# Kernel optimization log

Measured on AMD Instinct MI355X. Metric: run time of the kernel, lower is better.

The kernel has to match this reference:

```python
import jax, jax.numpy as jnp
import numpy as np
import math

B, T, D_MOTION = 2, 1536, 256
D_MODEL, N_HEADS, D_FF, N_LAYERS = 512, 8, 2048, 6
D_HEAD = D_MODEL // N_HEADS
FPS = 30
PERIOD = FPS // 2
CONTEXT_FRAMES = 10
NEG = -1e9  # large negative instead of -inf so fully-masked rows give uniform attn, not NaN


def _w(k, shape, fan_in):
    return jax.random.normal(k, shape, jnp.float32) / np.sqrt(fan_in)


def setup_inputs() -> dict:
    key = jax.random.key(0)
    ks = jax.random.split(key, 16)
    L = N_LAYERS
    din = D_MOTION + 5 + 1
    inp = {
        'motion': jax.random.normal(ks[0], (B, T, D_MOTION), jnp.float32),
        'traj': jax.random.normal(ks[1], (B, T, 5), jnp.float32),
        'me_w1': _w(ks[2], (din, D_MODEL), din), 'me_b1': jnp.zeros((D_MODEL,), jnp.float32),
        'me_w2': _w(ks[3], (D_MODEL, D_MODEL), D_MODEL), 'me_b2': jnp.zeros((D_MODEL,), jnp.float32),
        'wq': _w(ks[4], (L, D_MODEL, D_MODEL), D_MODEL), 'bq': jnp.zeros((L, D_MODEL), jnp.float32),
        'wk': _w(ks[5], (L, D_MODEL, D_MODEL), D_MODEL), 'bk': jnp.zeros((L, D_MODEL), jnp.float32),
        'wv': _w(ks[6], (L, D_MODEL, D_MODEL), D_MODEL), 'bv': jnp.zeros((L, D_MODEL), jnp.float32),
        'wo': _w(ks[7], (L, D_MODEL, D_MODEL), D_MODEL), 'bo': jnp.zeros((L, D_MODEL), jnp.float32),
        'ln1_g': jnp.ones((L, D_MODEL), jnp.float32), 'ln1_b': jnp.zeros((L, D_MODEL), jnp.float32),
        'ffn_w1': _w(ks[8], (L, D_MODEL, D_FF), D_MODEL), 'ffn_b1': jnp.zeros((L, D_FF), jnp.float32),
        'ffn_w2': _w(ks[9], (L, D_FF, D_MODEL), D_FF), 'ffn_b2': jnp.zeros((L, D_MODEL), jnp.float32),
        'ln2_g': jnp.ones((L, D_MODEL), jnp.float32), 'ln2_b': jnp.zeros((L, D_MODEL), jnp.float32),
        'fln_g': jnp.ones((D_MODEL,), jnp.float32), 'fln_b': jnp.zeros((D_MODEL,), jnp.float32),
        'dec_w1': _w(ks[10], (D_MODEL, D_MODEL), D_MODEL), 'dec_b1': jnp.zeros((D_MODEL,), jnp.float32),
        'dec_w2': _w(ks[11], (D_MODEL, D_MOTION), D_MODEL), 'dec_b2': jnp.zeros((D_MOTION,), jnp.float32),
    }
    return inp


def _layer_norm(x, g, b):
    m = jnp.mean(x, axis=-1, keepdims=True)
    v = jnp.mean((x - m) ** 2, axis=-1, keepdims=True)
    return (x - m) * jax.lax.rsqrt(v + 1e-5) * g + b


def _leaky(x):
    return jnp.where(x >= 0, x, 0.01 * x)


def _forward(motion, traj, me_w1, me_b1, me_w2, me_b2, wq, bq, wk, bk, wv, bv, wo, bo,
             ln1_g, ln1_b, ffn_w1, ffn_b1, ffn_w2, ffn_b2, ln2_g, ln2_b,
             fln_g, fln_b, dec_w1, dec_b1, dec_w2, dec_b2):
    idx = jnp.arange(T)
    dist = jnp.abs(idx[:, None] - idx[None, :])                       # [T,T]
    atten_bias = -(dist // PERIOD).astype(jnp.float32)                # periodic distance bias

    # context mask: keep first context_frames and last frame
    batch_mask = jnp.ones((T, 1), jnp.float32).at[CONTEXT_FRAMES:-1].set(0.0)
    mask = jnp.broadcast_to(batch_mask[None], (B, T, 1))              # [B,T,1]
    cf = jnp.ones((T,), bool).at[CONTEXT_FRAMES:-1].set(False)        # constrained frames

    original_motion = motion
    motion = motion * mask

    # motion encoder (dropout inactive at eval)
    h = jnp.concatenate([motion, traj, mask], axis=-1)                # [B,T,D_MOTION+6]
    x = _leaky(h @ me_w1 + me_b1)
    x = _leaky(x @ me_w2 + me_b2)

    # periodic positional embedding (sinusoidal on pos mod period)
    pos = jnp.mod(jnp.arange(T, dtype=jnp.float32), float(PERIOD))
    half = D_MODEL // 2
    div = jnp.exp(-np.log(10000.0) * (2.0 * jnp.arange(half, dtype=jnp.float32)) / D_MODEL)
    ang = pos[:, None] * div[None, :]
    pe = jnp.concatenate([jnp.sin(ang), jnp.cos(ang)], axis=-1)       # [T,D_MODEL]
    x = x + pe[None]

    # dynamically growing attention window
    num_trans = T - CONTEXT_FRAMES - 1
    ksz = math.ceil(num_trans / 2 / N_LAYERS) * 2 + 1
    kern = jnp.ones((ksz,), jnp.float32)
    thr = ksz // 2
    scale = 1.0 / np.sqrt(D_HEAD)

    for i in range(N_LAYERS):
        # attn mask: True = blocked
        amask = (dist > thr) | (~cf)[None, :]                         # [T,T]
        h = _layer_norm(x, ln1_g[i], ln1_b[i])                        # pre-layernorm
        q = (h @ wq[i] + bq[i]).reshape(B, T, N_HEADS, D_HEAD)
        k = (h @ wk[i] + bk[i]).reshape(B, T, N_HEADS, D_HEAD)
        v = (h @ wv[i] + bv[i]).reshape(B, T, N_HEADS, D_HEAD)
        scores = jnp.einsum('bqhd,bkhd->bhqk', q, k) * scale + atten_bias
        scores = jnp.where(amask[None, None], NEG, scores)
        attn = jax.nn.softmax(scores, axis=-1)
        out = jnp.einsum('bhqk,bkhd->bqhd', attn, v).reshape(B, T, D_MODEL)
        x = x + out @ wo[i] + bo[i]
        # position-wise FFN (pre-layernorm)
        h = _layer_norm(x, ln2_g[i], ln2_b[i])
        x = x + jax.nn.relu(h @ ffn_w1[i] + ffn_b1[i]) @ ffn_w2[i] + ffn_b2[i]
        # grow constrained frames by conv1d with ones kernel (same padding)
        cf = jnp.convolve(cf.astype(jnp.float32), kern, mode='same') > 0.5

    x = _layer_norm(x, fln_g, fln_b)
    x = _leaky(x @ dec_w1 + dec_b1)
    x = x @ dec_w2 + dec_b2                                           # [B,T,D_MOTION]
    out = original_motion * mask + x * (1.0 - mask)
    return out, mask


def reference(motion, traj, me_w1, me_b1, me_w2, me_b2, wq, bq, wk, bk, wv, bv, wo, bo,
              ln1_g, ln1_b, ffn_w1, ffn_b1, ffn_w2, ffn_b2, ln2_g, ln2_b,
              fln_g, fln_b, dec_w1, dec_b1, dec_w2, dec_b2):
    return _forward(motion, traj, me_w1, me_b1, me_w2, me_b2, wq, bq, wk, bk, wv, bv, wo, bo,
                    ln1_g, ln1_b, ffn_w1, ffn_b1, ffn_w2, ffn_b2, ln2_g, ln2_b,
                    fln_g, fln_b, dec_w1, dec_b1, dec_w2, dec_b2)
```

## Files before the change

### kernel.cpp

```cpp
#include <hip/hip_runtime.h>
#include <math.h>

typedef unsigned short ushort_t;
typedef unsigned int uint_t;
typedef __bf16 bf16x4 __attribute__((ext_vector_type(4)));
typedef __bf16 bf16x8 __attribute__((ext_vector_type(8)));
typedef float f32x4 __attribute__((ext_vector_type(4)));

#define T_SEQ   1536
#define NB      2
#define MROWS   3072
#define DMODEL  512
#define NHEADS  8
#define DHEAD   64
#define DFF     2048
#define DMOTION 256
#define NLAYERS 6
#define PERIODN 15
#define CTXF    10
#define THRW    128
#define KIN     384

__device__ __forceinline__ float bf2f(ushort_t u) { return __uint_as_float((uint_t)u << 16); }
__device__ __forceinline__ ushort_t f2bf(float f) {
    uint_t x = __float_as_uint(f);
    return (ushort_t)((x + 0x7fffu + ((x >> 16) & 1u)) >> 16);
}

__global__ __launch_bounds__(256) void pe_k(float* __restrict__ pe) {
    int idx = blockIdx.x * 256 + threadIdx.x;
    if (idx >= PERIODN * DMODEL) return;
    int p = idx / DMODEL, c = idx % DMODEL;
    int j = (c < DMODEL / 2) ? c : (c - DMODEL / 2);
    float div = __expf(-logf(10000.0f) * (2.0f * (float)j) / (float)DMODEL);
    float ang = (float)p * div;
    pe[idx] = (c < DMODEL / 2) ? sinf(ang) : cosf(ang);
}

__global__ __launch_bounds__(256) void build_k(const float* __restrict__ motion,
                                               const float* __restrict__ traj,
                                               ushort_t* __restrict__ hin,
                                               float* __restrict__ mask_out) {
    int idx = blockIdx.x * 256 + threadIdx.x;
    if (idx >= MROWS * KIN) return;
    int row = idx / KIN, c = idx % KIN;
    int t = row % T_SEQ;
    float mv = (t < CTXF || t == T_SEQ - 1) ? 1.0f : 0.0f;
    float val;
    if (c < DMOTION)            val = motion[(size_t)row * DMOTION + c] * mv;
    else if (c < DMOTION + 5)   val = traj[(size_t)row * 5 + (c - DMOTION)];
    else if (c == DMOTION + 5)  val = mv;
    else                        val = 0.0f;
    hin[idx] = f2bf(val);
    if (c == 0) mask_out[row] = mv;
}

__global__ __launch_bounds__(256)
void tconv_k(const float* __restrict__ src, size_t sstride,
             ushort_t* __restrict__ dst, size_t dstride,
             int K, int N, int Kpad) {
    __shared__ float t[32][33];
    src += (size_t)blockIdx.z * sstride;
    dst += (size_t)blockIdx.z * dstride;
    const int kb = blockIdx.y * 32, nb = blockIdx.x * 32;
    const int tx = threadIdx.x & 31, ty = threadIdx.x >> 5;
#pragma unroll
    for (int i = 0; i < 4; ++i) {
        int k = kb + ty + i * 8, n = nb + tx;
        t[ty + i * 8][tx] = (k < K && n < N) ? src[(size_t)k * N + n] : 0.0f;
    }
    __syncthreads();
#pragma unroll
    for (int i = 0; i < 4; ++i) {
        int n = nb + ty + i * 8, kk = kb + tx;
        if (n < N && kk < Kpad) dst[(size_t)n * Kpad + kk] = f2bf(t[tx][ty + i * 8]);
    }
}

__global__ __launch_bounds__(256)
void tconv_qkv_k(const float* __restrict__ wq, const float* __restrict__ wk,
                 const float* __restrict__ wv, ushort_t* __restrict__ qkvt) {
    __shared__ float t[32][33];
    const int z = blockIdx.z, s = z % 3, l = z / 3;
    const float* src = (s == 0 ? wq : s == 1 ? wk : wv) + (size_t)l * DMODEL * DMODEL;
    ushort_t* dst = qkvt + (size_t)z * DMODEL * DMODEL;
    const int kb = blockIdx.y * 32, nb = blockIdx.x * 32;
    const int tx = threadIdx.x & 31, ty = threadIdx.x >> 5;
#pragma unroll
    for (int i = 0; i < 4; ++i)
        t[ty + i * 8][tx] = src[(size_t)(kb + ty + i * 8) * DMODEL + nb + tx];
    __syncthreads();
#pragma unroll
    for (int i = 0; i < 4; ++i)
        dst[(size_t)(nb + ty + i * 8) * DMODEL + kb + tx] = f2bf(t[tx][ty + i * 8]);
}

__global__ __launch_bounds__(256)
void bcat_k(const float* __restrict__ bq, const float* __restrict__ bk,
            const float* __restrict__ bv, float* __restrict__ bqkv) {
    int idx = blockIdx.x * 256 + threadIdx.x;
    if (idx >= NLAYERS * 3 * DMODEL) return;
    int l = idx / (3 * DMODEL), n = idx % (3 * DMODEL);
    int s = n >> 9, c = n & 511;
    const float* b = (s == 0 ? bq : s == 1 ? bk : bv);
    bqkv[idx] = b[l * DMODEL + c];
}

#define SLD 136
#define CL  68
template <int ACT, bool RES, bool PE, bool OUTBF>
__global__ __launch_bounds__(256)
void sgemm_k(const ushort_t* __restrict__ A, int K,
             const ushort_t* __restrict__ Wt,
             const float* __restrict__ bias,
             const float* __restrict__ res,
             const float* __restrict__ pe15,
             void* __restrict__ Cout, int N) {
    __shared__ ushort_t As[32 * SLD];
    __shared__ ushort_t Bs[64 * SLD];
    const int tid = threadIdx.x;
    const int lane = tid & 63, wid = tid >> 6;
    const int m0 = blockIdx.y * 32, n0 = blockIdx.x * 64;
    const int l4 = lane >> 4, l15 = lane & 15;
    const int srow = tid >> 4, scol = (tid & 15) * 8;

    f32x4 acc[2][4];
#pragma unroll
    for (int m = 0; m < 2; ++m)
#pragma unroll
        for (int n = 0; n < 4; ++n) acc[m][n] = (f32x4){0.f, 0.f, 0.f, 0.f};

    const int niter = K >> 7;

    for (int it = 0; it < niter; ++it) {
        const int k0 = it << 7;
        const uint4 a0 = *(const uint4*)(A  + (size_t)(m0 + srow)      * K + k0 + scol);
        const uint4 a1 = *(const uint4*)(A  + (size_t)(m0 + 16 + srow) * K + k0 + scol);
        const uint4 b0 = *(const uint4*)(Wt + (size_t)(n0 + srow)      * K + k0 + scol);
        const uint4 b1 = *(const uint4*)(Wt + (size_t)(n0 + 16 + srow) * K + k0 + scol);
        const uint4 b2 = *(const uint4*)(Wt + (size_t)(n0 + 32 + srow) * K + k0 + scol);
        const uint4 b3 = *(const uint4*)(Wt + (size_t)(n0 + 48 + srow) * K + k0 + scol);
        __syncthreads();
        *(uint4*)&As[srow * SLD + scol]        = a0;
        *(uint4*)&As[(16 + srow) * SLD + scol] = a1;
        *(uint4*)&Bs[srow * SLD + scol]        = b0;
        *(uint4*)&Bs[(16 + srow) * SLD + scol] = b1;
        *(uint4*)&Bs[(32 + srow) * SLD + scol] = b2;
        *(uint4*)&Bs[(48 + srow) * SLD + scol] = b3;
        __syncthreads();

        const int kb = wid * 32;
        bf16x8 af[2], bf[4];
#pragma unroll
        for (int m = 0; m < 2; ++m) {
            const ushort_t* p = &As[(m * 16 + l15) * SLD + kb];
            bf16x4 lo4 = *(const bf16x4*)(p + l4 * 4);
            bf16x4 hi4 = *(const bf16x4*)(p + 16 + l4 * 4);
            af[m] = __builtin_shufflevector(lo4, hi4, 0, 1, 2, 3, 4, 5, 6, 7);
        }
#pragma unroll
        for (int n = 0; n < 4; ++n) {
            const ushort_t* p = &Bs[(n * 16 + l15) * SLD + kb];
            bf16x4 lo4 = *(const bf16x4*)(p + l4 * 4);
            bf16x4 hi4 = *(const bf16x4*)(p + 16 + l4 * 4);
            bf[n] = __builtin_shufflevector(lo4, hi4, 0, 1, 2, 3, 4, 5, 6, 7);
        }
#pragma unroll
        for (int m = 0; m < 2; ++m)
#pragma unroll
            for (int n = 0; n < 4; ++n)
                acc[m][n] = __builtin_amdgcn_mfma_f32_16x16x32_bf16(af[m], bf[n], acc[m][n], 0, 0, 0);
    }

    float* cb0 = (float*)As;
    float* cb1 = (float*)Bs;
    __syncthreads();
    if (wid >= 2) {
        float* cb = (wid == 2) ? cb0 : cb1;
#pragma unroll
        for (int m = 0; m < 2; ++m)
#pragma unroll
            for (int n = 0; n < 4; ++n)
#pragma unroll
                for (int r = 0; r < 4; ++r)
                    cb[(m * 16 + l4 * 4 + r) * CL + n * 16 + l15] = acc[m][n][r];
    }
    __syncthreads();
    if (wid < 2) {
        float* cb = (wid == 0) ? cb0 : cb1;
#pragma unroll
        for (int m = 0; m < 2; ++m)
#pragma unroll
            for (int n = 0; n < 4; ++n)
#pragma unroll
                for (int r = 0; r < 4; ++r)
                    cb[(m * 16 + l4 * 4 + r) * CL + n * 16 + l15] += acc[m][n][r];
    }
    __syncthreads();

    const int row = tid >> 3, c0 = (tid & 7) * 8;
    const int grow = m0 + row;
#pragma unroll
    for (int j = 0; j < 8; ++j) {
        const int gcol = n0 + c0 + j;
        float v = cb0[row * CL + c0 + j] + cb1[row * CL + c0 + j] + bias[gcol];
        if (ACT == 1) v = v >= 0.f ? v : 0.01f * v;
        else if (ACT == 2) v = fmaxf(v, 0.f);
        if (PE) v += pe15[((grow % T_SEQ) % PERIODN) * DMODEL + gcol];
        if (RES) v += res[(size_t)grow * N + gcol];
        if (OUTBF) ((ushort_t*)Cout)[(size_t)grow * N + gcol] = f2bf(v);
        else       ((float*)Cout)[(size_t)grow * N + gcol] = v;
    }
}

__global__ __launch_bounds__(256)
void ln_k(const float* __restrict__ X, const float* __restrict__ g,
          const float* __restrict__ b, ushort_t* __restrict__ Y) {
    const int wid = threadIdx.x >> 6, lane = threadIdx.x & 63;
    const int row = blockIdx.x * 4 + wid;
    const float* x = X + (size_t)row * DMODEL;
    float v[8], s = 0.f;
#pragma unroll
    for (int j = 0; j < 8; ++j) { v[j] = x[lane + 64 * j]; s += v[j]; }
#pragma unroll
    for (int o = 32; o; o >>= 1) s += __shfl_xor(s, o);
    const float mean = s * (1.0f / DMODEL);
    float vs = 0.f;
#pragma unroll
    for (int j = 0; j < 8; ++j) { float d = v[j] - mean; vs += d * d; }
#pragma unroll
    for (int o = 32; o; o >>= 1) vs += __shfl_xor(vs, o);
    const float inv = rsqrtf(vs * (1.0f / DMODEL) + 1e-5f);
    ushort_t* y = Y + (size_t)row * DMODEL;
#pragma unroll
    for (int j = 0; j < 8; ++j) {
        const int c = lane + 64 * j;
        y[c] = f2bf((v[j] - mean) * inv * g[c] + b[c]);
    }
}

__global__ __launch_bounds__(1024)
void vmeanp_k(const ushort_t* __restrict__ qkv, float* __restrict__ vmp) {
    __shared__ float red[16][64];
    const int bh = blockIdx.x, ch = blockIdx.y;
    const int b = bh >> 3, h = bh & 7;
    const int wid = threadIdx.x >> 6, lane = threadIdx.x & 63;
    const ushort_t* Vb = qkv + (size_t)(b * T_SEQ) * 1536 + 1024 + h * 64 + lane;
    float s = 0.f;
    const int t0 = ch * 192;
    for (int t = t0 + wid; t < t0 + 192; t += 16) s += bf2f(Vb[(size_t)t * 1536]);
    red[wid][lane] = s;
    __syncthreads();
    if (wid == 0) {
        float tot = 0.f;
#pragma unroll
        for (int i = 0; i < 16; ++i) tot += red[i][lane];
        vmp[(ch * 16 + bh) * 64 + lane] = tot;
    }
}

__global__ __launch_bounds__(1024)
void vmred_k(const float* __restrict__ vmp, float* __restrict__ vm) {
    const int t = threadIdx.x;
    float s = 0.f;
#pragma unroll
    for (int ch = 0; ch < 8; ++ch) s += vmp[ch * 1024 + t];
    vm[t] = s * (1.0f / T_SEQ);
}

__global__ __launch_bounds__(256)
void vfill_k(const float* __restrict__ vm, ushort_t* __restrict__ attout, int q0) {
    const int qrow = q0 + blockIdx.x, b = blockIdx.y;
    const int tid = threadIdx.x;
#pragma unroll
    for (int r = 0; r < 2; ++r) {
        const int c = tid + r * 256;
        attout[(size_t)(b * T_SEQ + qrow) * DMODEL + c] = f2bf(vm[b * 512 + c]);
    }
}

#define KLD 72
#define VLD 36
__global__ __launch_bounds__(256)
void attn3_k(const ushort_t* __restrict__ qkv, ushort_t* __restrict__ attout,
             int lo, int hi, int nlow, int qhi0, int tl, int st) {
    __shared__ ushort_t klds_[4][32 * KLD];
    __shared__ ushort_t vlds_[4][64 * VLD];
    const int lane = threadIdx.x & 63, wid = threadIdx.x >> 6;
    const int s = blockIdx.x * 4 + wid;
    if (s >= st) return;
    const int h = blockIdx.y, b = blockIdx.z;
    const int l15 = lane & 15, l4 = lane >> 4;

    int qb, qend;
    if (s < tl) { qb = 16 * s;                qend = nlow - 1; }
    else        { qb = qhi0 + 16 * (s - tl);  qend = T_SEQ - 1; }
    const int nr = qend - qb;

    ushort_t* klds = klds_[wid];
    ushort_t* vlds = vlds_[wid];
    const size_t rbase = (size_t)(b * T_SEQ) * 1536;
    const int q = qb + l15;

    const int qrow_r = min(q, T_SEQ - 1);
    const ushort_t* qptr = qkv + rbase + (size_t)qrow_r * 1536 + h * 64;
    bf16x8 bq[2];
#pragma unroll
    for (int kh = 0; kh < 2; ++kh) {
        bf16x4 lo4 = *(const bf16x4*)(qptr + kh * 32 + l4 * 4);
        bf16x4 hi4 = *(const bf16x4*)(qptr + kh * 32 + 16 + l4 * 4);
        bq[kh] = __builtin_shufflevector(lo4, hi4, 0, 1, 2, 3, 4, 5, 6, 7);
    }

    const int band0 = max(0, qb - THRW);
    const int band1 = min(T_SEQ - 1, qb + 15 + THRW);
    const int i1s = band0, i1e = min(band1, lo - 1);
    const int i2s = max(band0, hi), i2e = band1;

    f32x4 O[4] = {{0.f,0.f,0.f,0.f},{0.f,0.f,0.f,0.f},{0.f,0.f,0.f,0.f},{0.f,0.f,0.f,0.f}};
    float m = -3.0e38f, lsum = 0.f;

#pragma unroll 1
    for (int seg = 0; seg < 2; ++seg) {
        const int s0 = seg ? i2s : i1s, s1 = seg ? i2e : i1e;
#pragma unroll 1
        for (int c0 = s0; c0 <= s1; c0 += 32) {
#pragma unroll
            for (int i = 0; i < 4; ++i) {
                const int idx = i * 64 + lane;
                const int row = idx >> 3, c = (idx & 7) * 8;
                const int kr = min(c0 + row, T_SEQ - 1);
                const uint4 kv = *(const uint4*)(qkv + rbase + (size_t)kr * 1536 + 512 + h * 64 + c);
                *(uint4*)&klds[row * KLD + c] = kv;
                const uint4 vv = *(const uint4*)(qkv + rbase + (size_t)kr * 1536 + 1024 + h * 64 + c);
                const ushort_t* vp = (const ushort_t*)&vv;
#pragma unroll
                for (int d = 0; d < 8; ++d) vlds[(c + d) * VLD + row] = vp[d];
            }
            f32x4 sacc[2];
#pragma unroll
            for (int ks = 0; ks < 2; ++ks) {
                f32x4 a = {0.f, 0.f, 0.f, 0.f};
#pragma unroll
                for (int kh = 0; kh < 2; ++kh) {
                    const ushort_t* kp = &klds[(16 * ks + l15) * KLD + kh * 32];
                    bf16x4 lo4 = *(const bf16x4*)(kp + l4 * 4);
                    bf16x4 hi4 = *(const bf16x4*)(kp + 16 + l4 * 4);
                    bf16x8 ak = __builtin_shufflevector(lo4, hi4, 0, 1, 2, 3, 4, 5, 6, 7);
                    a = __builtin_amdgcn_mfma_f32_16x16x32_bf16(ak, bq[kh], a, 0, 0, 0);
                }
                sacc[ks] = a;
            }
            float sv[8];
            bool vld[8];
            float cm = -3.0e38f;
#pragma unroll
            for (int ks = 0; ks < 2; ++ks)
#pragma unroll
                for (int r = 0; r < 4; ++r) {
                    const int key = c0 + 16 * ks + 4 * l4 + r;
                    const int dist = (q > key) ? (q - key) : (key - q);
                    const bool v = (dist <= THRW) && (key < lo || key >= hi) && (key < T_SEQ);
                    const int ii = ks * 4 + r;
                    sv[ii] = sacc[ks][r] * 0.125f - (float)(dist / PERIODN);
                    vld[ii] = v;
                    cm = fmaxf(cm, v ? sv[ii] : -3.0e38f);
                }
            cm = fmaxf(cm, __shfl_xor(cm, 16));
            cm = fmaxf(cm, __shfl_xor(cm, 32));
            const float mnew = fmaxf(m, cm);
            const float sc = __expf(m - mnew);
            m = mnew;
            float p[8], psum = 0.f;
#pragma unroll
            for (int ii = 0; ii < 8; ++ii) {
                p[ii] = vld[ii] ? __expf(sv[ii] - mnew) : 0.f;
                psum += p[ii];
            }
            psum += __shfl_xor(psum, 16);
            psum += __shfl_xor(psum, 32);
            lsum = lsum * sc + psum;
#pragma unroll
            for (int ds = 0; ds < 4; ++ds) O[ds] *= sc;
            bf16x8 pb;
#pragma unroll
            for (int ii = 0; ii < 8; ++ii) pb[ii] = (__bf16)p[ii];
#pragma unroll
            for (int ds = 0; ds < 4; ++ds) {
                const ushort_t* vp2 = &vlds[(16 * ds + l15) * VLD];
                bf16x4 lo4 = *(const bf16x4*)(vp2 + 4 * l4);
                bf16x4 hi4 = *(const bf16x4*)(vp2 + 16 + 4 * l4);
                bf16x8 av = __builtin_shufflevector(lo4, hi4, 0, 1, 2, 3, 4, 5, 6, 7);
                O[ds] = __builtin_amdgcn_mfma_f32_16x16x32_bf16(av, pb, O[ds], 0, 0, 0);
            }
        }
    }
    if (l15 <= nr) {
        const float inv = 1.0f / lsum;
        ushort_t* op = attout + (size_t)(b * T_SEQ + qb + l15) * DMODEL + h * 64;
#pragma unroll
        for (int ds = 0; ds < 4; ++ds)
#pragma unroll
            for (int r = 0; r < 4; ++r)
                op[16 * ds + 4 * l4 + r] = f2bf(O[ds][r] * inv);
    }
}

__global__ __launch_bounds__(256)
void final_k(const float* __restrict__ motion, const float* __restrict__ xdec,
             float* __restrict__ out) {
    int idx = blockIdx.x * 256 + threadIdx.x;
    if (idx >= MROWS * DMOTION) return;
    const int row = idx >> 8;
    const int t = row % T_SEQ;
    const float mv = (t < CTXF || t == T_SEQ - 1) ? 1.0f : 0.0f;
    out[idx] = motion[idx] * mv + xdec[idx] * (1.0f - mv);
}

extern "C" void kernel_launch(void* const* d_in, const int* in_sizes, int n_in,
                              void* d_out, int out_size, void* d_ws, size_t ws_size,
                              hipStream_t stream) {
    const float* motion = (const float*)d_in[0];
    const float* traj   = (const float*)d_in[1];
    const float* me_w1  = (const float*)d_in[2];
    const float* me_b1  = (const float*)d_in[3];
    const float* me_w2  = (const float*)d_in[4];
    const float* me_b2  = (const float*)d_in[5];
    const float* wq = (const float*)d_in[6];
    const float* bq = (const float*)d_in[7];
    const float* wk = (const float*)d_in[8];
    const float* bk = (const float*)d_in[9];
    const float* wv = (const float*)d_in[10];
    const float* bv = (const float*)d_in[11];
    const float* wo = (const float*)d_in[12];
    const float* bo = (const float*)d_in[13];
    const float* ln1_g = (const float*)d_in[14];
    const float* ln1_b = (const float*)d_in[15];
    const float* ffn_w1 = (const float*)d_in[16];
    const float* ffn_b1 = (const float*)d_in[17];
    const float* ffn_w2 = (const float*)d_in[18];
    const float* ffn_b2 = (const float*)d_in[19];
    const float* ln2_g = (const float*)d_in[20];
    const float* ln2_b = (const float*)d_in[21];
    const float* fln_g = (const float*)d_in[22];
    const float* fln_b = (const float*)d_in[23];
    const float* dec_w1 = (const float*)d_in[24];
    const float* dec_b1 = (const float*)d_in[25];
    const float* dec_w2 = (const float*)d_in[26];
    const float* dec_b2 = (const float*)d_in[27];

    float* out = (float*)d_out;
    float* mask_out = out + (size_t)MROWS * DMOTION;

    char* base = (char*)d_ws;
    auto alloc = [&](size_t bytes) { char* p = base; base += (bytes + 255) & ~(size_t)255; return p; };

    ushort_t* qkvt  = (ushort_t*)alloc((size_t)NLAYERS * 1536 * 512 * 2);
    ushort_t* wot   = (ushort_t*)alloc((size_t)NLAYERS * 512 * 512 * 2);
    ushort_t* ffn1t = (ushort_t*)alloc((size_t)NLAYERS * 2048 * 512 * 2);
    ushort_t* ffn2t = (ushort_t*)alloc((size_t)NLAYERS * 512 * 2048 * 2);
    ushort_t* mew1t = (ushort_t*)alloc((size_t)512 * KIN * 2);
    ushort_t* mew2t = (ushort_t*)alloc((size_t)512 * 512 * 2);
    ushort_t* dec1t = (ushort_t*)alloc((size_t)512 * 512 * 2);
    ushort_t* dec2t = (ushort_t*)alloc((size_t)256 * 512 * 2);
    float*    bqkv  = (float*)alloc((size_t)NLAYERS * 1536 * 4);
    float*    pe15  = (float*)alloc((size_t)PERIODN * DMODEL * 4);
    float*    vmp   = (float*)alloc((size_t)8 * 16 * 64 * 4);
    float*    vm    = (float*)alloc((size_t)16 * 64 * 4);
    ushort_t* hin   = (ushort_t*)alloc((size_t)MROWS * KIN * 2);
    float*    x     = (float*)alloc((size_t)MROWS * DMODEL * 4);
    ushort_t* h     = (ushort_t*)alloc((size_t)MROWS * DMODEL * 2);
    ushort_t* qkv   = (ushort_t*)alloc((size_t)MROWS * 1536 * 2);
    ushort_t* ff    = (ushort_t*)alloc((size_t)MROWS * DFF * 2);
    float*    xdec  = (float*)qkv;

    const dim3 blk(256);
    pe_k<<<(PERIODN * DMODEL + 255) / 256, blk, 0, stream>>>(pe15);
    build_k<<<(MROWS * KIN + 255) / 256, blk, 0, stream>>>(motion, traj, hin, mask_out);

    tconv_qkv_k<<<dim3(16, 16, 18), blk, 0, stream>>>(wq, wk, wv, qkvt);
    tconv_k<<<dim3(16, 16, 6), blk, 0, stream>>>(wo, 512 * 512, wot, 512 * 512, 512, 512, 512);
    tconv_k<<<dim3(64, 16, 6), blk, 0, stream>>>(ffn_w1, 512 * 2048, ffn1t, 2048 * 512, 512, 2048, 512);
    tconv_k<<<dim3(16, 64, 6), blk, 0, stream>>>(ffn_w2, 2048 * 512, ffn2t, 512 * 2048, 2048, 512, 2048);
    tconv_k<<<dim3(16, 12, 1), blk, 0, stream>>>(me_w1, 0, mew1t, 0, 262, 512, KIN);
    tconv_k<<<dim3(16, 16, 1), blk, 0, stream>>>(me_w2, 0, mew2t, 0, 512, 512, 512);
    tconv_k<<<dim3(16, 16, 1), blk, 0, stream>>>(dec_w1, 0, dec1t, 0, 512, 512, 512);
    tconv_k<<<dim3(8, 16, 1),  blk, 0, stream>>>(dec_w2, 0, dec2t, 0, 512, 256, 512);
    bcat_k<<<(NLAYERS * 1536 + 255) / 256, blk, 0, stream>>>(bq, bk, bv, bqkv);

    const dim3 gs512(8, 96), gs1536(24, 96), gsff(32, 96), gs256(4, 96);

    sgemm_k<1, false, false, true ><<<gs512, blk, 0, stream>>>(hin, KIN, mew1t, me_b1, nullptr, nullptr, h, 512);
    sgemm_k<1, false, true,  false><<<gs512, blk, 0, stream>>>(h, 512, mew2t, me_b2, nullptr, pe15, x, 512);

    for (int i = 0; i < NLAYERS; ++i) {
        const int lo = CTXF + THRW * i;
        const int hi = (T_SEQ - 1) - THRW * i;
        int qlow_end = lo + 127;
        int qhi0 = hi - 128;
        int nlow, ninact;
        if (qhi0 <= qlow_end + 1) {
            nlow = T_SEQ; qhi0 = T_SEQ; ninact = 0;
        } else {
            nlow = qlow_end + 1;
            ninact = qhi0 - nlow;
        }
        const int tl2 = (nlow + 15) / 16;
        const int th2 = (T_SEQ - qhi0 + 15) / 16;
        const int st  = tl2 + th2;

        ln_k<<<MROWS / 4, blk, 0, stream>>>(x, ln1_g + i * 512, ln1_b + i * 512, h);
        sgemm_k<0, false, false, true><<<gs1536, blk, 0, stream>>>(h, 512, qkvt + (size_t)i * 1536 * 512, bqkv + i * 1536, nullptr, nullptr, qkv, 1536);
        if (ninact > 0) {
            vmeanp_k<<<dim3(16, 8), dim3(1024), 0, stream>>>(qkv, vmp);
            vmred_k<<<1, dim3(1024), 0, stream>>>(vmp, vm);
            vfill_k<<<dim3(ninact, NB), blk, 0, stream>>>(vm, h, nlow);
        }
        attn3_k<<<dim3((st + 3) / 4, NHEADS, NB), blk, 0, stream>>>(qkv, h, lo, hi, nlow, qhi0, tl2, st);
        sgemm_k<0, true, false, false><<<gs512, blk, 0, stream>>>(h, 512, wot + (size_t)i * 512 * 512, bo + i * 512, x, nullptr, x, 512);
        ln_k<<<MROWS / 4, blk, 0, stream>>>(x, ln2_g + i * 512, ln2_b + i * 512, h);
        sgemm_k<2, false, false, true><<<gsff, blk, 0, stream>>>(h, 512, ffn1t + (size_t)i * 2048 * 512, ffn_b1 + i * 2048, nullptr, nullptr, ff, 2048);
        sgemm_k<0, true, false, false><<<gs512, blk, 0, stream>>>(ff, 2048, ffn2t + (size_t)i * 512 * 2048, ffn_b2 + i * 512, x, nullptr, x, 512);
    }

    ln_k<<<MROWS / 4, blk, 0, stream>>>(x, fln_g, fln_b, h);
    sgemm_k<1, false, false, true ><<<gs512, blk, 0, stream>>>(h, 512, dec1t, dec_b1, nullptr, nullptr, ff, 512);
    sgemm_k<0, false, false, false><<<gs256, blk, 0, stream>>>(ff, 512, dec2t, dec_b2, nullptr, nullptr, xdec, 256);

    final_k<<<(MROWS * DMOTION + 255) / 256, blk, 0, stream>>>(motion, xdec, out);
}
```

Baseline: 818.2 us.

## Double-buffer GEMM tiles with direct global-to-LDS loads and XOR swizzle

Rewrites the GEMM main loop to stage A and W tiles straight into shared memory with global_load_lds, so data skips the register round-trip. Two LDS buffers let the next K-tile load while MFMAs run on the current one. An XOR swizzle replaces the padded row stride to avoid bank conflicts. This doubles the shared-memory footprint, which may lower occupancy, and it relies on async LDS loads being complete at the barrier.

```diff
diff --git a/kernel.cpp b/kernel.cpp
--- a/kernel.cpp
+++ b/kernel.cpp
@@ -25,6 +25,11 @@
 __device__ __forceinline__ ushort_t f2bf(float f) {
     uint_t x = __float_as_uint(f);
     return (ushort_t)((x + 0x7fffu + ((x >> 16) & 1u)) >> 16);
+}
+
+__device__ __forceinline__ void gl2lds(const ushort_t* g, ushort_t* l) {
+    __builtin_amdgcn_global_load_lds((const __attribute__((address_space(1))) void*)g,
+                                     (__attribute__((address_space(3))) void*)l, 16, 0, 0);
 }
 
 __global__ __launch_bounds__(256) void pe_k(float* __restrict__ pe) {
@@ -106,23 +111,22 @@
     bqkv[idx] = b[l * DMODEL + c];
 }
 
-#define SLD 136
 #define CL  68
 template <int ACT, bool RES, bool PE, bool OUTBF>
 __global__ __launch_bounds__(256)
-void sgemm_k(const ushort_t* __restrict__ A, int K,
+void qgemm_k(const ushort_t* __restrict__ A, int K,
              const ushort_t* __restrict__ Wt,
              const float* __restrict__ bias,
              const float* __restrict__ res,
              const float* __restrict__ pe15,
              void* __restrict__ Cout, int N) {
-    __shared__ ushort_t As[32 * SLD];
-    __shared__ ushort_t Bs[64 * SLD];
+    __shared__ ushort_t smem[2][(32 + 64) * 128];
     const int tid = threadIdx.x;
     const int lane = tid & 63, wid = tid >> 6;
     const int m0 = blockIdx.y * 32, n0 = blockIdx.x * 64;
     const int l4 = lane >> 4, l15 = lane & 15;
-    const int srow = tid >> 4, scol = (tid & 15) * 8;
+    const int lrow = lane >> 4;
+    const int lu   = lane & 15;
 
     f32x4 acc[2][4];
 #pragma unroll
@@ -132,49 +136,59 @@
 
     const int niter = K >> 7;
 
-    for (int it = 0; it < niter; ++it) {
-        const int k0 = it << 7;
-        const uint4 a0 = *(const uint4*)(A  + (size_t)(m0 + srow)      * K + k0 + scol);
-        const uint4 a1 = *(const uint4*)(A  + (size_t)(m0 + 16 + srow) * K + k0 + scol);
-        const uint4 b0 = *(const uint4*)(Wt + (size_t)(n0 + srow)      * K + k0 + scol);
-        const uint4 b1 = *(const uint4*)(Wt + (size_t)(n0 + 16 + srow) * K + k0 + scol);
-        const uint4 b2 = *(const uint4*)(Wt + (size_t)(n0 + 32 + srow) * K + k0 + scol);
-        const uint4 b3 = *(const uint4*)(Wt + (size_t)(n0 + 48 + srow) * K + k0 + scol);
-        __syncthreads();
-        *(uint4*)&As[srow * SLD + scol]        = a0;
-        *(uint4*)&As[(16 + srow) * SLD + scol] = a1;
-        *(uint4*)&Bs[srow * SLD + scol]        = b0;
-        *(uint4*)&Bs[(16 + srow) * SLD + scol] = b1;
-        *(uint4*)&Bs[(32 + srow) * SLD + scol] = b2;
-        *(uint4*)&Bs[(48 + srow) * SLD + scol] = b3;
-        __syncthreads();
-
-        const int kb = wid * 32;
+    auto stage = [&](int buf, int k0) {
+        ushort_t* dst = &smem[buf][0];
+#pragma unroll
+        for (int j = 0; j < 6; ++j) {
+            const int inst = wid * 6 + j;
+            if (inst < 8) {
+                const int row = inst * 4 + lrow;
+                const int u = lu ^ (row & 15);
+                gl2lds(A + (size_t)(m0 + row) * K + k0 + u * 8, dst + inst * 512);
+            } else {
+                const int bi = inst - 8;
+                const int row = bi * 4 + lrow;
+                const int u = lu ^ (row & 15);
+                gl2lds(Wt + (size_t)(n0 + row) * K + k0 + u * 8,
+                       dst + 32 * 128 + bi * 512);
+            }
+        }
+    };
+
+    const int kbyte = wid * 64;
+    auto rdfrag = [&](const ushort_t* t, int row) -> bf16x8 {
+        const int off0 = kbyte + l4 * 8;
+        const int off1 = kbyte + 32 + l4 * 8;
+        const int a0 = row * 256 + (((off0 & ~15) ^ ((row & 15) << 4)) | (off0 & 15));
+        const int a1 = row * 256 + (((off1 & ~15) ^ ((row & 15) << 4)) | (off1 & 15));
+        bf16x4 lo = *(const bf16x4*)((const char*)t + a0);
+        bf16x4 hi = *(const bf16x4*)((const char*)t + a1);
+        return __builtin_shufflevector(lo, hi, 0, 1, 2, 3, 4, 5, 6, 7);
+    };
+
+    stage(0, 0);
+    __syncthreads();
+    int cur = 0;
+    for (int t = 0; t < niter; ++t) {
+        if (t + 1 < niter) stage(cur ^ 1, (t + 1) << 7);
+        const ushort_t* As = &smem[cur][0];
+        const ushort_t* Bs = &smem[cur][32 * 128];
         bf16x8 af[2], bf[4];
 #pragma unroll
-        for (int m = 0; m < 2; ++m) {
-            const ushort_t* p = &As[(m * 16 + l15) * SLD + kb];
-            bf16x4 lo4 = *(const bf16x4*)(p + l4 * 4);
-            bf16x4 hi4 = *(const bf16x4*)(p + 16 + l4 * 4);
-            af[m] = __builtin_shufflevector(lo4, hi4, 0, 1, 2, 3, 4, 5, 6, 7);
-        }
-#pragma unroll
-        for (int n = 0; n < 4; ++n) {
-            const ushort_t* p = &Bs[(n * 16 + l15) * SLD + kb];
-            bf16x4 lo4 = *(const bf16x4*)(p + l4 * 4);
-            bf16x4 hi4 = *(const bf16x4*)(p + 16 + l4 * 4);
-            bf[n] = __builtin_shufflevector(lo4, hi4, 0, 1, 2, 3, 4, 5, 6, 7);
-        }
+        for (int m = 0; m < 2; ++m) af[m] = rdfrag(As, m * 16 + l15);
+#pragma unroll
+        for (int n = 0; n < 4; ++n) bf[n] = rdfrag(Bs, n * 16 + l15);
 #pragma unroll
         for (int m = 0; m < 2; ++m)
 #pragma unroll
             for (int n = 0; n < 4; ++n)
                 acc[m][n] = __builtin_amdgcn_mfma_f32_16x16x32_bf16(af[m], bf[n], acc[m][n], 0, 0, 0);
-    }
-
-    float* cb0 = (float*)As;
-    float* cb1 = (float*)Bs;
-    __syncthreads();
+        __syncthreads();
+        cur ^= 1;
+    }
+
+    float* cb0 = (float*)&smem[0][0];
+    float* cb1 = (float*)&smem[1][0];
     if (wid >= 2) {
         float* cb = (wid == 2) ? cb0 : cb1;
 #pragma unroll
@@ -490,8 +504,8 @@
 
     const dim3 gs512(8, 96), gs1536(24, 96), gsff(32, 96), gs256(4, 96);
 
-    sgemm_k<1, false, false, true ><<<gs512, blk, 0, stream>>>(hin, KIN, mew1t, me_b1, nullptr, nullptr, h, 512);
-    sgemm_k<1, false, true,  false><<<gs512, blk, 0, stream>>>(h, 512, mew2t, me_b2, nullptr, pe15, x, 512);
+    qgemm_k<1, false, false, true ><<<gs512, blk, 0, stream>>>(hin, KIN, mew1t, me_b1, nullptr, nullptr, h, 512);
+    qgemm_k<1, false, true,  false><<<gs512, blk, 0, stream>>>(h, 512, mew2t, me_b2, nullptr, pe15, x, 512);
 
     for (int i = 0; i < NLAYERS; ++i) {
         const int lo = CTXF + THRW * i;
@@ -510,22 +524,22 @@
         const int st  = tl2 + th2;
 
         ln_k<<<MROWS / 4, blk, 0, stream>>>(x, ln1_g + i * 512, ln1_b + i * 512, h);
-        sgemm_k<0, false, false, true><<<gs1536, blk, 0, stream>>>(h, 512, qkvt + (size_t)i * 1536 * 512, bqkv + i * 1536, nullptr, nullptr, qkv, 1536);
+        qgemm_k<0, false, false, true><<<gs1536, blk, 0, stream>>>(h, 512, qkvt + (size_t)i * 1536 * 512, bqkv + i * 1536, nullptr, nullptr, qkv, 1536);
         if (ninact > 0) {
             vmeanp_k<<<dim3(16, 8), dim3(1024), 0, stream>>>(qkv, vmp);
             vmred_k<<<1, dim3(1024), 0, stream>>>(vmp, vm);
             vfill_k<<<dim3(ninact, NB), blk, 0, stream>>>(vm, h, nlow);
         }
         attn3_k<<<dim3((st + 3) / 4, NHEADS, NB), blk, 0, stream>>>(qkv, h, lo, hi, nlow, qhi0, tl2, st);
-        sgemm_k<0, true, false, false><<<gs512, blk, 0, stream>>>(h, 512, wot + (size_t)i * 512 * 512, bo + i * 512, x, nullptr, x, 512);
+        qgemm_k<0, true, false, false><<<gs512, blk, 0, stream>>>(h, 512, wot + (size_t)i * 512 * 512, bo + i * 512, x, nullptr, x, 512);
         ln_k<<<MROWS / 4, blk, 0, stream>>>(x, ln2_g + i * 512, ln2_b + i * 512, h);
-        sgemm_k<2, false, false, true><<<gsff, blk, 0, stream>>>(h, 512, ffn1t + (size_t)i * 2048 * 512, ffn_b1 + i * 2048, nullptr, nullptr, ff, 2048);
-        sgemm_k<0, true, false, false><<<gs512, blk, 0, stream>>>(ff, 2048, ffn2t + (size_t)i * 512 * 2048, ffn_b2 + i * 512, x, nullptr, x, 512);
+        qgemm_k<2, false, false, true><<<gsff, blk, 0, stream>>>(h, 512, ffn1t + (size_t)i * 2048 * 512, ffn_b1 + i * 2048, nullptr, nullptr, ff, 2048);
+        qgemm_k<0, true, false, false><<<gs512, blk, 0, stream>>>(ff, 2048, ffn2t + (size_t)i * 512 * 2048, ffn_b2 + i * 512, x, nullptr, x, 512);
     }
 
     ln_k<<<MROWS / 4, blk, 0, stream>>>(x, fln_g, fln_b, h);
-    sgemm_k<1, false, false, true ><<<gs512, blk, 0, stream>>>(h, 512, dec1t, dec_b1, nullptr, nullptr, ff, 512);
-    sgemm_k<0, false, false, false><<<gs256, blk, 0, stream>>>(ff, 512, dec2t, dec_b2, nullptr, nullptr, xdec, 256);
+    qgemm_k<1, false, false, true ><<<gs512, blk, 0, stream>>>(h, 512, dec1t, dec_b1, nullptr, nullptr, ff, 512);
+    qgemm_k<0, false, false, false><<<gs256, blk, 0, stream>>>(ff, 512, dec2t, dec_b2, nullptr, nullptr, xdec, 256);
 
     final_k<<<(MROWS * DMOTION + 255) / 256, blk, 0, stream>>>(motion, xdec, out);
 }
```

Measured after the change: 813.4 us. Within noise of the previous version (-0.6%).
